# Kernel tuning notes

Hardware: AMD Instinct MI355X
Metric: run time of the kernel (lower is better)

Reference implementation:

```python
import jax, jax.numpy as jnp
from jax import lax
import numpy as np

THRESHOLD = 0.9
KHALF = 5  # conv_kernel_size; full conv width = 2*KHALF + 1 = 11


def _cif_scan(eouts, alpha_norm, elens, ylens, Lp1):
    """Vectorized-over-batch integrate-and-fire scan over time (lax.scan)."""
    B, T, D = eouts.shape
    bidx = jnp.arange(B)
    dt = eouts.dtype

    def step(carry, xs):
        alpha_accum, state, n_tok, fired = carry
        a_t, e_t, t = xs  # a_t: [B], e_t: [B,D], t: scalar int
        alpha_accum = alpha_accum + a_t
        active = (t <= elens - 1) & (n_tok < ylens)
        fire = active & (alpha_accum >= THRESHOLD)
        ak1 = 1.0 - alpha_accum
        ak2 = a_t - ak1
        # attention-weight column for time t
        aw_col = jnp.zeros((B, Lp1), dt)
        w_old = jnp.where(fire, ak1, jnp.where(active, a_t, jnp.zeros((), dt)))
        aw_col = aw_col.at[bidx, n_tok].add(w_old)
        n_new = n_tok + fire.astype(n_tok.dtype)
        aw_col = aw_col.at[bidx, n_new].add(jnp.where(fire, ak2, jnp.zeros((), dt)))
        # fired output row (set once per token slot)
        fire_val = state + ak1[:, None] * e_t
        cur = fired[bidx, n_tok]
        fired = fired.at[bidx, n_tok].set(jnp.where(fire[:, None], fire_val, cur))
        # integrate / reset state
        state = jnp.where(fire[:, None], ak2[:, None] * e_t,
                          jnp.where(active[:, None], state + a_t[:, None] * e_t, state))
        alpha_accum = jnp.where(fire, ak2, alpha_accum)
        return (alpha_accum, state, n_new, fired), aw_col

    init = (jnp.zeros((B,), dt), jnp.zeros((B, D), dt),
            jnp.zeros((B,), jnp.int32), jnp.zeros((B, Lp1, D), dt))
    xs = (jnp.swapaxes(alpha_norm, 0, 1), jnp.swapaxes(eouts, 0, 1),
          jnp.arange(T))
    (_, _, _, fired), aw_cols = lax.scan(step, init, xs)
    aws = jnp.transpose(aw_cols, (1, 2, 0))[:, None]  # [B,1,Lp1,T]
    return fired, aws


def _forward(eouts, conv_w, conv_b, proj_w, proj_b, elens, ylens, L):
    # Conv1d over time, 'same' padding: [B,T,D] -> [B,T,C]
    conv_feat = lax.conv_general_dilated(
        eouts, conv_w, window_strides=(1,), padding=[(KHALF, KHALF)],
        dimension_numbers=('NWC', 'WIO', 'NWC')) + conv_b
    alpha = jax.nn.sigmoid(conv_feat @ proj_w + proj_b)[:, :, 0]  # [B,T]
    alpha_norm = alpha / jnp.sum(alpha, axis=1, keepdims=True) \
        * ylens[:, None].astype(alpha.dtype)
    fired, aws = _cif_scan(eouts, alpha_norm, elens, ylens, L + 1)
    return fired[:, :L], alpha, aws


def setup_inputs():
    key = jax.random.key(0)
    k1, k2, k3, k4, k5 = jax.random.split(key, 5)
    B, T, D, C = 16, 2048, 512, 512
    eouts = jax.random.normal(k1, (B, T, D), jnp.float32)
    elens = jnp.maximum(jax.random.randint(k2, (B,), 0, T), T // 2).astype(jnp.int32)
    ylens = jnp.maximum(jax.random.randint(k3, (B,), 0, 128), 32).astype(jnp.int32)
    conv_w = jax.random.normal(k4, (2 * KHALF + 1, D, C), jnp.float32) * 0.02
    conv_b = jnp.zeros((C,), jnp.float32)
    proj_w = jax.random.normal(k5, (C, 1), jnp.float32) * 0.05
    proj_b = jnp.zeros((1,), jnp.float32)
    return dict(eouts=eouts, conv_w=conv_w, conv_b=conv_b,
                proj_w=proj_w, proj_b=proj_b, elens=elens, ylens=ylens)


def reference(eouts, conv_w, conv_b, proj_w, proj_b, elens, ylens):
    L = int(jnp.max(ylens))  # max_len = ylens.max(), as in the original
    return _forward(eouts, conv_w, conv_b, proj_w, proj_b, elens, ylens, L)
```

## Files before the change

### kernel.cpp

```cpp
#include <hip/hip_runtime.h>
#include <math.h>

#define KHALF 5
#define MAXF 256

__global__ void k_weff(const float* __restrict__ conv_w, const float* __restrict__ conv_b,
                       const float* __restrict__ proj_w, const float* __restrict__ proj_b,
                       float* __restrict__ w_eff, float* __restrict__ b_eff,
                       int KD, int C) {
    int gid = blockIdx.x * blockDim.x + threadIdx.x;
    int wave = gid >> 6;
    int lane = gid & 63;
    if (wave > KD) return;
    float s = 0.f;
    if (wave < KD) {
        const float* row = conv_w + (size_t)wave * C;
        for (int c = lane * 4; c < C; c += 256) {
            float4 v = *reinterpret_cast<const float4*>(row + c);
            float4 w = *reinterpret_cast<const float4*>(proj_w + c);
            s += v.x * w.x + v.y * w.y + v.z * w.z + v.w * w.w;
        }
    } else {
        for (int c = lane; c < C; c += 64) s += conv_b[c] * proj_w[c];
    }
#pragma unroll
    for (int off = 32; off > 0; off >>= 1) s += __shfl_down(s, off, 64);
    if (lane == 0) {
        if (wave < KD) w_eff[wave] = s;
        else           b_eff[0] = s + proj_b[0];
    }
}

__global__ __launch_bounds__(256) void k_qdot(const float* __restrict__ eouts,
                                              const float* __restrict__ w_eff,
                                              float* __restrict__ q, int BT) {
    __shared__ float tile[64 * 132];
    __shared__ float part[64 * 49];
    const int u0 = blockIdx.x * 64;
    const int lane = threadIdx.x & 63;
    const int s = __builtin_amdgcn_readfirstlane(threadIdx.x >> 6);
    float acc[11];
#pragma unroll
    for (int k = 0; k < 11; ++k) acc[k] = 0.f;
    for (int c = 0; c < 4; ++c) {
        __syncthreads();
#pragma unroll
        for (int it = 0; it < 8; ++it) {
            int idx = it * 256 + threadIdx.x;
            int r = idx >> 5, j4 = idx & 31;
            float4 v = *reinterpret_cast<const float4*>(
                eouts + (size_t)(u0 + r) * 512 + c * 128 + j4 * 4);
            *reinterpret_cast<float4*>(&tile[r * 132 + j4 * 4]) = v;
        }
        __syncthreads();
#pragma unroll
        for (int j4 = 0; j4 < 8; ++j4) {
            float4 av = *reinterpret_cast<const float4*>(&tile[lane * 132 + s * 32 + j4 * 4]);
            int dg = c * 128 + s * 32 + j4 * 4;
#pragma unroll
            for (int k = 0; k < 11; ++k) {
                float4 wv = *reinterpret_cast<const float4*>(w_eff + k * 512 + dg);
                acc[k] += av.x * wv.x + av.y * wv.y + av.z * wv.z + av.w * wv.w;
            }
        }
    }
#pragma unroll
    for (int k = 0; k < 11; ++k) part[lane * 49 + s * 12 + k] = acc[k];
    __syncthreads();
    if (threadIdx.x < 64) {
        int r = threadIdx.x;
        const float* p = &part[r * 49];
        float o[12];
#pragma unroll
        for (int k = 0; k < 11; ++k)
            o[k] = (p[k] + p[12 + k]) + (p[24 + k] + p[36 + k]);
        o[11] = 0.f;
        float4* dst = reinterpret_cast<float4*>(q + (size_t)(u0 + r) * 12);
        dst[0] = make_float4(o[0], o[1], o[2], o[3]);
        dst[1] = make_float4(o[4], o[5], o[6], o[7]);
        dst[2] = make_float4(o[8], o[9], o[10], o[11]);
    }
}

__global__ __launch_bounds__(256) void k_sigpart(const float* __restrict__ q,
                                                 const float* __restrict__ b_eff,
                                                 float* __restrict__ alpha,
                                                 float* __restrict__ partials,
                                                 int T, int tcb) {
    __shared__ float qs[266 * 12];
    __shared__ float psm[4];
    int bx = blockIdx.x;
    int b = bx / tcb, tc = bx % tcb;
    int t0 = tc * 256;
    const float* qb = q + (size_t)b * T * 12;
    const int base = (t0 - 5) * 12;
    const int lim = T * 12;
    for (int i = threadIdx.x; i < 266 * 12; i += 256) {
        int gi = base + i;
        qs[i] = (gi >= 0 && gi < lim) ? qb[gi] : 0.f;
    }
    __syncthreads();
    int t = t0 + threadIdx.x;
    float sacc = b_eff[0];
#pragma unroll
    for (int k = 0; k < 11; ++k) sacc += qs[(threadIdx.x + k) * 12 + k];
    float al = 1.f / (1.f + expf(-sacc));
    alpha[(size_t)b * T + t] = al;
    float s = al;
    int lane = threadIdx.x & 63;
    int w = threadIdx.x >> 6;
#pragma unroll
    for (int off = 32; off > 0; off >>= 1) s += __shfl_down(s, off, 64);
    if (lane == 0) psm[w] = s;
    __syncthreads();
    if (threadIdx.x == 0) {
        float tot = 0.f;
        for (int i = 0; i < 4; ++i) tot += psm[i];
        partials[bx] = tot;
    }
}

__global__ void k_alpha(const float* __restrict__ eouts,
                        const float* __restrict__ w_eff,
                        const float* __restrict__ b_eff,
                        float* __restrict__ alpha,
                        int B, int T, int D) {
    const int W = 2 * KHALF + 1;
    int gid = blockIdx.x * blockDim.x + threadIdx.x;
    int wave = gid >> 6;
    int lane = gid & 63;
    if (wave >= B * T) return;
    int b = wave / T;
    int t = wave - b * T;
    int WD = W * D;
    int t0 = t - KHALF;
    float s = 0.f;
    if (t0 >= 0 && t0 + W <= T) {
        const float* base = eouts + ((size_t)b * T + t0) * D;
        for (int j = lane * 4; j < WD; j += 256) {
            float4 v = *reinterpret_cast<const float4*>(base + j);
            float4 w = *reinterpret_cast<const float4*>(w_eff + j);
            s += v.x * w.x + v.y * w.y + v.z * w.z + v.w * w.w;
        }
    } else {
        const float* base = eouts + (size_t)b * T * D;
        for (int j = lane; j < WD; j += 64) {
            int tt = t0 + j / D;
            if (tt >= 0 && tt < T) {
                int d = j - (j / D) * D;
                s += base[(size_t)tt * D + d] * w_eff[j];
            }
        }
    }
#pragma unroll
    for (int off = 32; off > 0; off >>= 1) s += __shfl_down(s, off, 64);
    if (lane == 0) {
        float logit = s + b_eff[0];
        alpha[(size_t)b * T + t] = 1.f / (1.f + expf(-logit));
    }
}

__global__ void k_chain(const float* __restrict__ alpha_in,
                        int use_part,
                        const float* __restrict__ partials, int npart,
                        const int* __restrict__ elens,
                        const int* __restrict__ ylens,
                        float* __restrict__ alpha_sum,
                        int* __restrict__ n_fired,
                        int* __restrict__ fire_t,
                        float* __restrict__ fire_a1,
                        float* __restrict__ fire_a2,
                        int T, int Lp1) {
    extern __shared__ float an[];
    __shared__ float sm[16];
    __shared__ float stot;
    int b = blockIdx.x;
    const float* row = alpha_in + (size_t)b * T;
    for (int i = threadIdx.x; i < T; i += blockDim.x) an[i] = row[i];
    __syncthreads();
    if (use_part) {
        if (threadIdx.x == 0) {
            float tot = 0.f;
            for (int i = 0; i < npart; ++i) tot += partials[b * npart + i];
            stot = tot;
            alpha_sum[b] = tot;
        }
    } else {
        float s = 0.f;
        for (int i = threadIdx.x; i < T; i += blockDim.x) s += an[i];
        int lane0 = threadIdx.x & 63;
        int w0 = threadIdx.x >> 6;
#pragma unroll
        for (int off = 32; off > 0; off >>= 1) s += __shfl_down(s, off, 64);
        if (lane0 == 0) sm[w0] = s;
        __syncthreads();
        if (threadIdx.x == 0) {
            float tot = 0.f;
            int nw = blockDim.x >> 6;
            for (int i = 0; i < nw; ++i) tot += sm[i];
            stot = tot;
            alpha_sum[b] = tot;
        }
    }
    __syncthreads();
    float ssum = stot;
    float yl = (float)ylens[b];
    for (int i = threadIdx.x; i < T; i += blockDim.x) an[i] = an[i] / ssum * yl;
    __syncthreads();
    if (threadIdx.x >= 64) return;
    int lane = threadIdx.x;

    int elen = elens[b];
    if (elen > T) elen = T;
    const int ylen = ylens[b];
    int* __restrict__ ft = fire_t + (size_t)b * Lp1;
    float* __restrict__ fa1 = fire_a1 + (size_t)b * Lp1;
    float* __restrict__ fa2 = fire_a2 + (size_t)b * Lp1;

    float accum = 0.f;
    int n = 0;
    bool done = false;
    for (int t0 = 0; t0 < elen && !done; t0 += 64) {
        int nv = elen - t0;
        if (nv > 64) nv = 64;
        float a = (lane < nv) ? an[t0 + lane] : 0.f;
        float P = a;
#pragma unroll
        for (int off = 1; off < 64; off <<= 1) {
            float tmp = __shfl_up(P, off, 64);
            if (lane >= off) P += tmp;
        }
        unsigned long long validmask =
            (nv == 64) ? ~0ull : ((1ull << nv) - 1ull);
        float base = accum;
        int start = 0;
        while (true) {
            bool cond = (base + P >= 0.9f);
            unsigned long long bal = __ballot(cond) & validmask;
            if (start > 0) bal &= (~0ull) << start;
            if (bal == 0) break;
            int u = __builtin_ctzll(bal);
            float Pu = __shfl(P, u, 64);
            float au = __shfl(a, u, 64);
            float accum_f = base + Pu;
            float ak1 = 1.f - accum_f;
            float ak2 = au - ak1;
            if (lane == 0) {
                ft[n] = t0 + u;
                fa1[n] = ak1;
                fa2[n] = ak2;
            }
            ++n;
            if (n >= ylen) { done = true; break; }
            base = ak2 - Pu;
            start = u + 1;
            if (start >= nv) break;
        }
        if (!done) {
            float Plast = __shfl(P, nv - 1, 64);
            accum = base + Plast;
        }
    }
    if (lane == 0) n_fired[b] = n;
}

__global__ void k_awfired(const float* __restrict__ eouts,
                          const float* __restrict__ alpha,
                          const float* __restrict__ alpha_sum,
                          const int* __restrict__ elens,
                          const int* __restrict__ ylens,
                          const int* __restrict__ n_fired,
                          const int* __restrict__ fire_t,
                          const float* __restrict__ fire_a1,
                          const float* __restrict__ fire_a2,
                          float* __restrict__ aws,
                          float* __restrict__ fired,
                          int T, int D, int L, int Lp1,
                          int AB, int tcpb, int DB) {
    if ((int)blockIdx.x < AB) {
        __shared__ int fts[MAXF];
        __shared__ float a1s[MAXF];
        __shared__ float a2s[MAXF];
        int b = blockIdx.x / tcpb;
        int tc = blockIdx.x % tcpb;
        int nf = n_fired[b];
        for (int i = threadIdx.x; i < nf; i += blockDim.x) {
            fts[i] = fire_t[(size_t)b * Lp1 + i];
            a1s[i] = fire_a1[(size_t)b * Lp1 + i];
            a2s[i] = fire_a2[(size_t)b * Lp1 + i];
        }
        __syncthreads();
        int t = tc * 256 + threadIdx.x;
        if (t >= T) return;
        int elen = elens[b];
        if (elen > T) elen = T;
        int ylen = ylens[b];
        bool active = (t < elen);
        int rowi = 0;
        bool isfire = false;
        float v1 = 0.f, v2 = 0.f;
        if (active) {
            int lo = 0, hi = nf;
            while (lo < hi) {
                int mid = (lo + hi) >> 1;
                if (fts[mid] < t) lo = mid + 1; else hi = mid;
            }
            rowi = lo;
            isfire = (rowi < nf && fts[rowi] == t);
            if (isfire) { v1 = a1s[rowi]; v2 = a2s[rowi]; }
            else if (rowi < ylen) v1 = alpha[(size_t)b * T + t] / alpha_sum[b] * (float)ylen;
            else active = false;
        }
        float* col = aws + (size_t)b * Lp1 * T + t;
        for (int r = 0; r < Lp1; ++r) {
            float v = 0.f;
            if (active) {
                if (r == rowi) v = v1;
                else if (isfire && r == rowi + 1) v = v2;
            }
            col[(size_t)r * T] = v;
        }
    } else {
        int idx = blockIdx.x - AB;
        int b = idx / (L * DB);
        int rem = idx % (L * DB);
        int n = rem / DB;
        int d = (rem % DB) * 256 + threadIdx.x;
        if (d >= D) return;
        int nf = n_fired[b];
        float* dst = fired + ((size_t)b * L + n) * D + d;
        if (n >= nf) { *dst = 0.f; return; }
        int t0 = (n == 0) ? 0 : fire_t[(size_t)b * Lp1 + n - 1];
        int t1 = fire_t[(size_t)b * Lp1 + n];
        float ak1 = fire_a1[(size_t)b * Lp1 + n];
        float ak2p = (n > 0) ? fire_a2[(size_t)b * Lp1 + n - 1] : 0.f;
        float ssum = alpha_sum[b];
        float yl = (float)ylens[b];
        const float* e = eouts + ((size_t)b * T + t0) * D + d;
        float accv = 0.f;
        for (int t = t0; t <= t1; ++t, e += D) {
            float wgt;
            if (t == t1) wgt = ak1;
            else if (t == t0 && n > 0) wgt = ak2p;
            else wgt = alpha[(size_t)b * T + t] / ssum * yl;
            accv += wgt * e[0];
        }
        *dst = accv;
    }
}

extern "C" void kernel_launch(void* const* d_in, const int* in_sizes, int n_in,
                              void* d_out, int out_size, void* d_ws, size_t ws_size,
                              hipStream_t stream) {
    const float* eouts  = (const float*)d_in[0];
    const float* conv_w = (const float*)d_in[1];
    const float* conv_b = (const float*)d_in[2];
    const float* proj_w = (const float*)d_in[3];
    const float* proj_b = (const float*)d_in[4];
    const int*   elens  = (const int*)d_in[5];
    const int*   ylens  = (const int*)d_in[6];

    const int B = in_sizes[5];
    const int C = in_sizes[2];
    const int W = 2 * KHALF + 1;
    const int D = in_sizes[1] / (W * C);
    const int T = in_sizes[0] / (B * D);
    const int L = (out_size - 2 * B * T) / (B * (D + T));
    const int Lp1 = L + 1;
    const int BT = B * T;
    const int tcb = T / 256;

    float* out   = (float*)d_out;
    float* fired = out;
    float* alpha = out + (size_t)B * L * D;
    float* aws   = alpha + (size_t)B * T;

    char*  ws        = (char*)d_ws;
    float* w_eff     = (float*)ws;
    float* b_eff     = (float*)(ws + (size_t)W * D * 4);
    float* alpha_sum = b_eff + 16;
    int*   n_fired   = (int*)(alpha_sum + B + 16);
    int*   fire_t    = n_fired + B + 16;
    float* fire_a1   = (float*)(fire_t + (size_t)B * Lp1 + 16);
    float* fire_a2   = fire_a1 + (size_t)B * Lp1 + 16;
    float* qbuf      = fire_a2 + (size_t)B * Lp1 + 16;
    float* partials  = qbuf + (size_t)BT * 12 + 16;
    size_t ws_need   = (size_t)((char*)(partials + (size_t)B * tcb + 16) - ws);

    const int KD = W * D;
    {
        long long threads = (long long)(KD + 1) * 64;
        int blocks = (int)((threads + 255) / 256);
        k_weff<<<blocks, 256, 0, stream>>>(conv_w, conv_b, proj_w, proj_b,
                                           w_eff, b_eff, KD, C);
    }

    const bool fast = (ws_size >= ws_need) && (D == 512) &&
                      (BT % 64 == 0) && (T % 256 == 0);
    if (fast) {
        k_qdot<<<BT / 64, 256, 0, stream>>>(eouts, w_eff, qbuf, BT);
        k_sigpart<<<B * tcb, 256, 0, stream>>>(qbuf, b_eff, alpha, partials, T, tcb);
    } else {
        long long threads = (long long)BT * 64;
        int blocks = (int)((threads + 255) / 256);
        k_alpha<<<blocks, 256, 0, stream>>>(eouts, w_eff, b_eff, alpha, B, T, D);
    }

    k_chain<<<B, 256, T * sizeof(float), stream>>>(
        alpha, fast ? 1 : 0, partials, tcb,
        elens, ylens, alpha_sum,
        n_fired, fire_t, fire_a1, fire_a2, T, Lp1);

    {
        int tcpb = (T + 255) / 256;
        int AB = B * tcpb;
        int DB = (D + 255) / 256;
        int FB = B * L * DB;
        k_awfired<<<AB + FB, 256, 0, stream>>>(eouts, alpha, alpha_sum,
                                               elens, ylens, n_fired,
                                               fire_t, fire_a1, fire_a2,
                                               aws, fired, T, D, L, Lp1,
                                               AB, tcpb, DB);
    }
}
```

Baseline: 196.7 us.

## Fuse all pipeline stages into one cooperative persistent kernel with grid syncs

```diff
diff --git a/kernel.cpp b/kernel.cpp
--- a/kernel.cpp
+++ b/kernel.cpp
@@ -1,8 +1,12 @@
 #include <hip/hip_runtime.h>
+#include <hip/hip_cooperative_groups.h>
 #include <math.h>
+
+namespace cg = cooperative_groups;
 
 #define KHALF 5
 #define MAXF 256
+
 
 __global__ void k_weff(const float* __restrict__ conv_w, const float* __restrict__ conv_b,
                        const float* __restrict__ proj_w, const float* __restrict__ proj_b,
@@ -209,14 +213,12 @@
     __syncthreads();
     if (threadIdx.x >= 64) return;
     int lane = threadIdx.x;
-
     int elen = elens[b];
     if (elen > T) elen = T;
     const int ylen = ylens[b];
     int* __restrict__ ft = fire_t + (size_t)b * Lp1;
     float* __restrict__ fa1 = fire_a1 + (size_t)b * Lp1;
     float* __restrict__ fa2 = fire_a2 + (size_t)b * Lp1;
-
     float accum = 0.f;
     int n = 0;
     bool done = false;
@@ -230,8 +232,7 @@
             float tmp = __shfl_up(P, off, 64);
             if (lane >= off) P += tmp;
         }
-        unsigned long long validmask =
-            (nv == 64) ? ~0ull : ((1ull << nv) - 1ull);
+        unsigned long long validmask = (nv == 64) ? ~0ull : ((1ull << nv) - 1ull);
         float base = accum;
         int start = 0;
         while (true) {
@@ -245,11 +246,7 @@
             float accum_f = base + Pu;
             float ak1 = 1.f - accum_f;
             float ak2 = au - ak1;
-            if (lane == 0) {
-                ft[n] = t0 + u;
-                fa1[n] = ak1;
-                fa2[n] = ak2;
-            }
+            if (lane == 0) { ft[n] = t0 + u; fa1[n] = ak1; fa2[n] = ak2; }
             ++n;
             if (n >= ylen) { done = true; break; }
             base = ak2 - Pu;
@@ -349,6 +346,291 @@
     }
 }
 
+struct MegaArgs {
+    const float *eouts, *conv_w, *conv_b, *proj_w, *proj_b;
+    const int *elens, *ylens;
+    float *w_eff, *b_eff, *alpha_sum;
+    int *n_fired, *fire_t;
+    float *fire_a1, *fire_a2, *qbuf, *partials;
+    float *fired, *alpha, *aws;
+    int B, T, D, C, L, Lp1, tcb, BT;
+};
+
+__global__ __launch_bounds__(256, 2) void k_mega(MegaArgs a) {
+    cg::grid_group gridg = cg::this_grid();
+    __shared__ __align__(16) char smem[29952];
+    const int lane = threadIdx.x & 63;
+
+    {
+        const int KD = 11 * a.D;
+        int gwave = (int)((blockIdx.x * 256 + threadIdx.x) >> 6);
+        int nw = (int)gridDim.x * 4;
+        for (int wv = gwave; wv <= KD; wv += nw) {
+            float s = 0.f;
+            if (wv < KD) {
+                const float* row = a.conv_w + (size_t)wv * a.C;
+                for (int c = lane * 4; c < a.C; c += 256) {
+                    float4 v = *reinterpret_cast<const float4*>(row + c);
+                    float4 w = *reinterpret_cast<const float4*>(a.proj_w + c);
+                    s += v.x * w.x + v.y * w.y + v.z * w.z + v.w * w.w;
+                }
+            } else {
+                for (int c = lane; c < a.C; c += 64) s += a.conv_b[c] * a.proj_w[c];
+            }
+#pragma unroll
+            for (int off = 32; off > 0; off >>= 1) s += __shfl_down(s, off, 64);
+            if (lane == 0) {
+                if (wv < KD) a.w_eff[wv] = s;
+                else         a.b_eff[0] = s + a.proj_b[0];
+            }
+        }
+    }
+    __threadfence();
+    gridg.sync();
+
+    {
+        float* tile = (float*)smem;
+        float* part = tile + 64 * 68;
+        const int sw = threadIdx.x >> 6;
+        const int ntile = a.BT >> 6;
+        for (int tl = blockIdx.x; tl < ntile; tl += gridDim.x) {
+            const int u0 = tl << 6;
+            float acc[11];
+#pragma unroll
+            for (int k = 0; k < 11; ++k) acc[k] = 0.f;
+            for (int c = 0; c < 8; ++c) {
+                __syncthreads();
+#pragma unroll
+                for (int it = 0; it < 4; ++it) {
+                    int idx = it * 256 + threadIdx.x;
+                    int r = idx >> 4, j4 = idx & 15;
+                    float4 v = *reinterpret_cast<const float4*>(
+                        a.eouts + (size_t)(u0 + r) * 512 + c * 64 + j4 * 4);
+                    *reinterpret_cast<float4*>(&tile[r * 68 + j4 * 4]) = v;
+                }
+                __syncthreads();
+#pragma unroll
+                for (int j4 = 0; j4 < 4; ++j4) {
+                    float4 av = *reinterpret_cast<const float4*>(&tile[lane * 68 + sw * 16 + j4 * 4]);
+                    int dg = c * 64 + sw * 16 + j4 * 4;
+#pragma unroll
+                    for (int k = 0; k < 11; ++k) {
+                        float4 wv = *reinterpret_cast<const float4*>(a.w_eff + k * 512 + dg);
+                        acc[k] += av.x * wv.x + av.y * wv.y + av.z * wv.z + av.w * wv.w;
+                    }
+                }
+            }
+            __syncthreads();
+#pragma unroll
+            for (int k = 0; k < 11; ++k) part[lane * 49 + sw * 12 + k] = acc[k];
+            __syncthreads();
+            if (threadIdx.x < 64) {
+                int r = threadIdx.x;
+                const float* p = &part[r * 49];
+                float o[12];
+#pragma unroll
+                for (int k = 0; k < 11; ++k)
+                    o[k] = (p[k] + p[12 + k]) + (p[24 + k] + p[36 + k]);
+                o[11] = 0.f;
+                float4* dst = reinterpret_cast<float4*>(a.qbuf + (size_t)(u0 + r) * 12);
+                dst[0] = make_float4(o[0], o[1], o[2], o[3]);
+                dst[1] = make_float4(o[4], o[5], o[6], o[7]);
+                dst[2] = make_float4(o[8], o[9], o[10], o[11]);
+            }
+        }
+    }
+    __threadfence();
+    gridg.sync();
+
+    for (int bx = blockIdx.x; bx < a.B * a.tcb; bx += gridDim.x) {
+        float* qs = (float*)smem;
+        float* psm = qs + 266 * 12;
+        int b = bx / a.tcb, tc = bx % a.tcb;
+        int t0 = tc * 256;
+        const float* qb = a.qbuf + (size_t)b * a.T * 12;
+        const int base = (t0 - 5) * 12;
+        const int lim = a.T * 12;
+        __syncthreads();
+        for (int i = threadIdx.x; i < 266 * 12; i += 256) {
+            int gi = base + i;
+            qs[i] = (gi >= 0 && gi < lim) ? qb[gi] : 0.f;
+        }
+        __syncthreads();
+        int t = t0 + threadIdx.x;
+        float sacc = a.b_eff[0];
+#pragma unroll
+        for (int k = 0; k < 11; ++k) sacc += qs[(threadIdx.x + k) * 12 + k];
+        float al = 1.f / (1.f + expf(-sacc));
+        a.alpha[(size_t)b * a.T + t] = al;
+        float s = al;
+        int w = threadIdx.x >> 6;
+#pragma unroll
+        for (int off = 32; off > 0; off >>= 1) s += __shfl_down(s, off, 64);
+        if (lane == 0) psm[w] = s;
+        __syncthreads();
+        if (threadIdx.x == 0) {
+            float tot = 0.f;
+            for (int i = 0; i < 4; ++i) tot += psm[i];
+            a.partials[bx] = tot;
+        }
+    }
+    __threadfence();
+    gridg.sync();
+
+    for (int b = blockIdx.x; b < a.B; b += gridDim.x) {
+        float* an = (float*)smem;
+        float* ssh = an + a.T;
+        const float* row = a.alpha + (size_t)b * a.T;
+        __syncthreads();
+        for (int i = threadIdx.x; i < a.T; i += 256) an[i] = row[i];
+        if (threadIdx.x == 0) {
+            float tot = 0.f;
+            for (int i = 0; i < a.tcb; ++i) tot += a.partials[b * a.tcb + i];
+            ssh[0] = tot;
+            a.alpha_sum[b] = tot;
+        }
+        __syncthreads();
+        float ssum = ssh[0];
+        float yl = (float)a.ylens[b];
+        for (int i = threadIdx.x; i < a.T; i += 256) an[i] = an[i] / ssum * yl;
+        __syncthreads();
+        if (threadIdx.x < 64) {
+            int elen = a.elens[b];
+            if (elen > a.T) elen = a.T;
+            const int ylen = a.ylens[b];
+            int* ft = a.fire_t + (size_t)b * a.Lp1;
+            float* fa1 = a.fire_a1 + (size_t)b * a.Lp1;
+            float* fa2 = a.fire_a2 + (size_t)b * a.Lp1;
+            float accum = 0.f;
+            int n = 0;
+            bool done = false;
+            for (int t0 = 0; t0 < elen && !done; t0 += 64) {
+                int nv = elen - t0;
+                if (nv > 64) nv = 64;
+                float av = (lane < nv) ? an[t0 + lane] : 0.f;
+                float P = av;
+#pragma unroll
+                for (int off = 1; off < 64; off <<= 1) {
+                    float tmp = __shfl_up(P, off, 64);
+                    if (lane >= off) P += tmp;
+                }
+                unsigned long long validmask = (nv == 64) ? ~0ull : ((1ull << nv) - 1ull);
+                float base = accum;
+                int start = 0;
+                while (true) {
+                    bool cond = (base + P >= 0.9f);
+                    unsigned long long bal = __ballot(cond) & validmask;
+                    if (start > 0) bal &= (~0ull) << start;
+                    if (bal == 0) break;
+                    int u = __builtin_ctzll(bal);
+                    float Pu = __shfl(P, u, 64);
+                    float au = __shfl(av, u, 64);
+                    float accum_f = base + Pu;
+                    float ak1 = 1.f - accum_f;
+                    float ak2 = au - ak1;
+                    if (lane == 0) { ft[n] = t0 + u; fa1[n] = ak1; fa2[n] = ak2; }
+                    ++n;
+                    if (n >= ylen) { done = true; break; }
+                    base = ak2 - Pu;
+                    start = u + 1;
+                    if (start >= nv) break;
+                }
+                if (!done) {
+                    float Plast = __shfl(P, nv - 1, 64);
+                    accum = base + Plast;
+                }
+            }
+            if (lane == 0) a.n_fired[b] = n;
+        }
+    }
+    __threadfence();
+    gridg.sync();
+
+    {
+        const int AB = a.B * a.tcb;
+        const int DB = (a.D + 255) / 256;
+        const int total = AB + a.B * a.L * DB;
+        int* fts = (int*)smem;
+        float* a1s = (float*)(fts + MAXF);
+        float* a2s = a1s + MAXF;
+        for (int task = blockIdx.x; task < total; task += gridDim.x) {
+            if (task < AB) {
+                int b = task / a.tcb;
+                int tc = task % a.tcb;
+                int nf = a.n_fired[b];
+                __syncthreads();
+                for (int i = threadIdx.x; i < nf; i += 256) {
+                    fts[i] = a.fire_t[(size_t)b * a.Lp1 + i];
+                    a1s[i] = a.fire_a1[(size_t)b * a.Lp1 + i];
+                    a2s[i] = a.fire_a2[(size_t)b * a.Lp1 + i];
+                }
+                __syncthreads();
+                int t = tc * 256 + threadIdx.x;
+                if (t < a.T) {
+                    int elen = a.elens[b];
+                    if (elen > a.T) elen = a.T;
+                    int ylen = a.ylens[b];
+                    bool active = (t < elen);
+                    int rowi = 0;
+                    bool isfire = false;
+                    float v1 = 0.f, v2 = 0.f;
+                    if (active) {
+                        int lo = 0, hi = nf;
+                        while (lo < hi) {
+                            int mid = (lo + hi) >> 1;
+                            if (fts[mid] < t) lo = mid + 1; else hi = mid;
+                        }
+                        rowi = lo;
+                        isfire = (rowi < nf && fts[rowi] == t);
+                        if (isfire) { v1 = a1s[rowi]; v2 = a2s[rowi]; }
+                        else if (rowi < ylen)
+                            v1 = a.alpha[(size_t)b * a.T + t] / a.alpha_sum[b] * (float)ylen;
+                        else active = false;
+                    }
+                    float* col = a.aws + (size_t)b * a.Lp1 * a.T + t;
+                    for (int r = 0; r < a.Lp1; ++r) {
+                        float v = 0.f;
+                        if (active) {
+                            if (r == rowi) v = v1;
+                            else if (isfire && r == rowi + 1) v = v2;
+                        }
+                        col[(size_t)r * a.T] = v;
+                    }
+                }
+            } else {
+                int idx = task - AB;
+                int b = idx / (a.L * DB);
+                int rem = idx % (a.L * DB);
+                int n = rem / DB;
+                int d = (rem % DB) * 256 + threadIdx.x;
+                if (d < a.D) {
+                    int nf = a.n_fired[b];
+                    float* dst = a.fired + ((size_t)b * a.L + n) * a.D + d;
+                    if (n >= nf) { *dst = 0.f; }
+                    else {
+                        int t0 = (n == 0) ? 0 : a.fire_t[(size_t)b * a.Lp1 + n - 1];
+                        int t1 = a.fire_t[(size_t)b * a.Lp1 + n];
+                        float ak1 = a.fire_a1[(size_t)b * a.Lp1 + n];
+                        float ak2p = (n > 0) ? a.fire_a2[(size_t)b * a.Lp1 + n - 1] : 0.f;
+                        float ssum = a.alpha_sum[b];
+                        float yl = (float)a.ylens[b];
+                        const float* e = a.eouts + ((size_t)b * a.T + t0) * a.D + d;
+                        float accv = 0.f;
+                        for (int t = t0; t <= t1; ++t, e += a.D) {
+                            float wgt;
+                            if (t == t1) wgt = ak1;
+                            else if (t == t0 && n > 0) wgt = ak2p;
+                            else wgt = a.alpha[(size_t)b * a.T + t] / ssum * yl;
+                            accv += wgt * e[0];
+                        }
+                        *dst = accv;
+                    }
+                }
+            }
+        }
+    }
+}
+
 extern "C" void kernel_launch(void* const* d_in, const int* in_sizes, int n_in,
                               void* d_out, int out_size, void* d_ws, size_t ws_size,
                               hipStream_t stream) {
@@ -368,7 +650,7 @@
     const int L = (out_size - 2 * B * T) / (B * (D + T));
     const int Lp1 = L + 1;
     const int BT = B * T;
-    const int tcb = T / 256;
+    const int tcb = (T + 255) / 256;
 
     float* out   = (float*)d_out;
     float* fired = out;
@@ -387,39 +669,64 @@
     float* partials  = qbuf + (size_t)BT * 12 + 16;
     size_t ws_need   = (size_t)((char*)(partials + (size_t)B * tcb + 16) - ws);
 
-    const int KD = W * D;
-    {
-        long long threads = (long long)(KD + 1) * 64;
-        int blocks = (int)((threads + 255) / 256);
-        k_weff<<<blocks, 256, 0, stream>>>(conv_w, conv_b, proj_w, proj_b,
-                                           w_eff, b_eff, KD, C);
-    }
-
-    const bool fast = (ws_size >= ws_need) && (D == 512) &&
-                      (BT % 64 == 0) && (T % 256 == 0);
+    const bool fast = (ws_size >= ws_need) && (D == 512) && (C == 512) &&
+                      (BT % 64 == 0) && (T % 256 == 0) && (T <= 7424) &&
+                      (Lp1 <= MAXF);
+
+    bool coop_done = false;
     if (fast) {
-        k_qdot<<<BT / 64, 256, 0, stream>>>(eouts, w_eff, qbuf, BT);
-        k_sigpart<<<B * tcb, 256, 0, stream>>>(qbuf, b_eff, alpha, partials, T, tcb);
-    } else {
-        long long threads = (long long)BT * 64;
-        int blocks = (int)((threads + 255) / 256);
-        k_alpha<<<blocks, 256, 0, stream>>>(eouts, w_eff, b_eff, alpha, B, T, D);
-    }
-
-    k_chain<<<B, 256, T * sizeof(float), stream>>>(
-        alpha, fast ? 1 : 0, partials, tcb,
-        elens, ylens, alpha_sum,
-        n_fired, fire_t, fire_a1, fire_a2, T, Lp1);
-
-    {
-        int tcpb = (T + 255) / 256;
-        int AB = B * tcpb;
-        int DB = (D + 255) / 256;
-        int FB = B * L * DB;
-        k_awfired<<<AB + FB, 256, 0, stream>>>(eouts, alpha, alpha_sum,
-                                               elens, ylens, n_fired,
-                                               fire_t, fire_a1, fire_a2,
-                                               aws, fired, T, D, L, Lp1,
-                                               AB, tcpb, DB);
+        int dev = 0, nCU = 0, coopAttr = 0, occ = 0;
+        hipGetDevice(&dev);
+        hipDeviceGetAttribute(&nCU, hipDeviceAttributeMultiprocessorCount, dev);
+        hipDeviceGetAttribute(&coopAttr, hipDeviceAttributeCooperativeLaunch, dev);
+        hipOccupancyMaxActiveBlocksPerMultiprocessor(&occ, (const void*)k_mega, 256, 0);
+        int maxBlk = occ * nCU;
+        int nblk = BT / 64;
+        if (nblk > maxBlk) nblk = maxBlk;
+        if (coopAttr && nblk >= B && nblk >= 64) {
+            MegaArgs a = { eouts, conv_w, conv_b, proj_w, proj_b, elens, ylens,
+                           w_eff, b_eff, alpha_sum, n_fired, fire_t,
+                           fire_a1, fire_a2, qbuf, partials,
+                           fired, alpha, aws,
+                           B, T, D, C, L, Lp1, tcb, BT };
+            void* kargs[] = { (void*)&a };
+            hipError_t e = hipLaunchCooperativeKernel((const void*)k_mega, dim3(nblk),
+                                                      dim3(256), kargs, 0, stream);
+            if (e == hipSuccess) coop_done = true;
+            else (void)hipGetLastError();
+        }
+    }
+
+    if (!coop_done) {
+        const int KD = W * D;
+        {
+            long long threads = (long long)(KD + 1) * 64;
+            int blocks = (int)((threads + 255) / 256);
+            k_weff<<<blocks, 256, 0, stream>>>(conv_w, conv_b, proj_w, proj_b,
+                                               w_eff, b_eff, KD, C);
+        }
+        if (fast) {
+            k_qdot<<<BT / 64, 256, 0, stream>>>(eouts, w_eff, qbuf, BT);
+            k_sigpart<<<B * tcb, 256, 0, stream>>>(qbuf, b_eff, alpha, partials, T, tcb);
+        } else {
+            long long threads = (long long)BT * 64;
+            int blocks = (int)((threads + 255) / 256);
+            k_alpha<<<blocks, 256, 0, stream>>>(eouts, w_eff, b_eff, alpha, B, T, D);
+        }
+        k_chain<<<B, 256, T * sizeof(float), stream>>>(
+            alpha, fast ? 1 : 0, partials, tcb,
+            elens, ylens, alpha_sum,
+            n_fired, fire_t, fire_a1, fire_a2, T, Lp1);
+        {
+            int tcpb = (T + 255) / 256;
+            int AB = B * tcpb;
+            int DB = (D + 255) / 256;
+            int FB = B * L * DB;
+            k_awfired<<<AB + FB, 256, 0, stream>>>(eouts, alpha, alpha_sum,
+                                                   elens, ylens, n_fired,
+                                                   fire_t, fire_a1, fire_a2,
+                                                   aws, fired, T, D, L, Lp1,
+                                                   AB, tcpb, DB);
+        }
     }
 }
```

Result: slower. 505.5 us (+157.0%).
